# Optimization experiments

Hardware: AMD Instinct MI355X
Metric: run time of the kernel (lower is better)

Reference implementation:

```python
import jax, jax.numpy as jnp
import numpy as np

H_IN = 1024
H_OUT = 1024
P = 512
DT_MIN = 0.004
DT_MAX = 0.1
STEP_RESCALE = 1.0
MIN_NEG = 1e-3
EPS_LAM = 1e-6
EPS_DIV = 1e-9
CLIP_MAX = 20.0


def _hippo_lambda_raw(p):
    # Mirrors TorchS5.__init__ HiPPO-LegS-style symmetric init.
    idx = np.arange(p, dtype=np.float64)
    Pv = np.sqrt(1.0 + 2.0 * idx)
    A = np.tril(Pv[:, None] * Pv[None, :]) - np.diag(idx)
    A = -A
    Pr = np.sqrt(idx + 0.5)
    S = A + Pr[:, None] * Pr[None, :]
    S_sym = 0.5 * (S + S.T)
    eig = np.linalg.eigvalsh(S_sym).astype(np.float32)
    lambda_init = -np.clip(np.abs(eig), 1e-3, None)
    raw = -np.log(np.expm1(np.clip(-lambda_init, 1e-6, None)))
    return jnp.asarray(raw, dtype=jnp.float32)


def setup_inputs() -> dict:
    key = jax.random.key(0)
    ku, kt, kb, kc = jax.random.split(key, 4)
    Bsz, L = 16, 1024
    u = jax.random.normal(ku, (Bsz, L, H_IN), dtype=jnp.float32)
    timesteps = jax.random.uniform(kt, (Bsz, L), dtype=jnp.float32)
    Lambda_raw = _hippo_lambda_raw(P)
    log_step_init = 0.5 * (np.log(DT_MIN) + np.log(DT_MAX))
    log_step = jnp.full((P,), log_step_init, dtype=jnp.float32)
    # kaiming_uniform_(a=sqrt(5)) -> U(-1/sqrt(fan_in), 1/sqrt(fan_in))
    Bmat = jax.random.uniform(kb, (P, H_IN), dtype=jnp.float32,
                              minval=-1.0, maxval=1.0) / np.sqrt(H_IN)
    Cmat = jax.random.uniform(kc, (H_OUT, P), dtype=jnp.float32,
                              minval=-1.0, maxval=1.0) / np.sqrt(P)
    Dvec = jnp.zeros((H_IN,), dtype=jnp.float32)  # H_in == H_out path
    return {"u": u, "timesteps": timesteps, "Lambda_raw": Lambda_raw,
            "log_step": log_step, "B": Bmat, "C": Cmat, "D": Dvec}


def reference(u, timesteps, Lambda_raw, log_step, B, C, D):
    # u: [B,L,H_in], timesteps: [B,L]
    Bu = jnp.einsum('ph,blh->blp', B, u)                      # [B,L,P]
    step_vec = STEP_RESCALE * jnp.exp(log_step)               # [P]
    Lam = -(jax.nn.softplus(Lambda_raw) + MIN_NEG)            # [P]
    Delta = jnp.maximum(step_vec[None, None, :] * timesteps[..., None], 0.0)
    A_bar = jnp.exp(jnp.minimum(Lam[None, None, :] * Delta, CLIP_MAX))
    # zoh gamma: (exp(Lam*Delta)-1)/Lam, fallback Delta near Lam=0
    gamma = jnp.where(jnp.abs(Lam)[None, None, :] > EPS_LAM,
                      (A_bar - 1.0) / Lam[None, None, :], Delta)
    b_seq = gamma * Bu
    A_cum = jnp.cumprod(A_bar, axis=1)                        # [B,L,P]
    z = b_seq / (A_cum + EPS_DIV)
    s = jnp.cumsum(z, axis=1)
    x_seq = A_cum * s
    ys = jnp.einsum('hp,blp->blh', C, x_seq) + D * u          # [B,L,H_out]
    return ys
```

## Files before the change

kernel.cpp:

```cpp
#include <hip/hip_runtime.h>
#include <cstdint>
#include <cstddef>

#define H_IN   1024
#define H_OUTD 1024
#define PDIM   512
#define BSZ    16
#define LSEQ   1024
#define BLM    (BSZ * LSEQ)
#define CCH    32
#define CLEN   32

typedef __bf16 bf16_t;
typedef __bf16 bf16x8 __attribute__((ext_vector_type(8)));
typedef float  floatx4 __attribute__((ext_vector_type(4)));

__device__ __forceinline__ unsigned short f2bf(float f) {
    unsigned u = __float_as_uint(f);
    u = u + 0x7fffu + ((u >> 16) & 1u);
    return (unsigned short)(u >> 16);
}
__device__ __forceinline__ float bf2f(unsigned short s) {
    return __uint_as_float((unsigned)s << 16);
}

__device__ __forceinline__ void gl_lds16(const void* g, void* l) {
    __builtin_amdgcn_global_load_lds(
        (const __attribute__((address_space(1))) void*)g,
        (__attribute__((address_space(3))) void*)l, 16, 0, 0);
}

__global__ void setup_kernel(const float* __restrict__ Lraw,
                             const float* __restrict__ lstep,
                             float* __restrict__ stepv,
                             float* __restrict__ lamv,
                             const float4* __restrict__ Bsrc,
                             ushort4* __restrict__ Bdst,
                             const float4* __restrict__ Csrc,
                             ushort4* __restrict__ Cdst) {
    const int gid = blockIdx.x * 256 + threadIdx.x;
    if (gid < PDIM) {
        stepv[gid] = expf(lstep[gid]);
        float x = Lraw[gid];
        float sp = fmaxf(x, 0.0f) + log1pf(expf(-fabsf(x)));
        lamv[gid] = -(sp + 1e-3f);
    }
    const int nB = PDIM * H_IN / 4;
    if (gid < nB) {
        float4 v = Bsrc[gid];
        ushort4 o;
        o.x = f2bf(v.x); o.y = f2bf(v.y); o.z = f2bf(v.z); o.w = f2bf(v.w);
        Bdst[gid] = o;
    } else {
        const int g2 = gid - nB;
        float4 v = Csrc[g2];
        ushort4 o;
        o.x = f2bf(v.x); o.y = f2bf(v.y); o.z = f2bf(v.z); o.w = f2bf(v.w);
        Cdst[g2] = o;
    }
}

__global__ void cvt_kernel(const float4* __restrict__ src,
                           ushort4* __restrict__ dst, int n4) {
    int i = blockIdx.x * blockDim.x + threadIdx.x;
    if (i < n4) {
        float4 v = src[i];
        ushort4 o;
        o.x = f2bf(v.x); o.y = f2bf(v.y); o.z = f2bf(v.z); o.w = f2bf(v.w);
        dst[i] = o;
    }
}

template<int EPI, int OUTBF>
__global__ __launch_bounds__(256, 4)
void gemm_nt(const bf16_t* __restrict__ A, const bf16_t* __restrict__ Bm,
             float* __restrict__ Cf, unsigned short* __restrict__ Cb,
             int M, int N, int K,
             const float* __restrict__ Dv, const unsigned short* __restrict__ U) {
    __shared__ bf16_t As[128 * 32];
    __shared__ bf16_t Bs[128 * 32];

    const int tid  = threadIdx.x;
    const int lane = tid & 63;
    const int w    = tid >> 6;
    const int m0   = blockIdx.y << 7;
    const int n0   = blockIdx.x << 7;
    const int wm   = (w & 1) << 6;
    const int wn   = (w >> 1) << 6;
    const int r16  = lane & 15;
    const int q    = lane >> 4;
    const int fsw  = (q ^ (r16 & 3)) << 3;

    const int srow = lane >> 2;
    const int seg  = (lane & 3) ^ (srow & 3);
    const int c0   = w * 32;
    const int c1   = c0 + 16;

    const bf16_t* gA0 = A  + (size_t)(m0 + c0 + srow) * K + seg * 8;
    const bf16_t* gA1 = A  + (size_t)(m0 + c1 + srow) * K + seg * 8;
    const bf16_t* gB0 = Bm + (size_t)(n0 + c0 + srow) * K + seg * 8;
    const bf16_t* gB1 = Bm + (size_t)(n0 + c1 + srow) * K + seg * 8;
    bf16_t* lA0 = &As[c0 * 32];
    bf16_t* lA1 = &As[c1 * 32];
    bf16_t* lB0 = &Bs[c0 * 32];
    bf16_t* lB1 = &Bs[c1 * 32];

    floatx4 acc[4][4] = {};

    for (int k0 = 0; k0 < K; k0 += 32) {
        gl_lds16(gA0 + k0, lA0);
        gl_lds16(gA1 + k0, lA1);
        gl_lds16(gB0 + k0, lB0);
        gl_lds16(gB1 + k0, lB1);
        __syncthreads();

        bf16x8 af[4], bfr[4];
#pragma unroll
        for (int i = 0; i < 4; ++i) {
            af[i]  = *(const bf16x8*)&As[(wm + i * 16 + r16) * 32 + fsw];
            bfr[i] = *(const bf16x8*)&Bs[(wn + i * 16 + r16) * 32 + fsw];
        }
#pragma unroll
        for (int mi = 0; mi < 4; ++mi)
#pragma unroll
            for (int ni = 0; ni < 4; ++ni)
                acc[mi][ni] = __builtin_amdgcn_mfma_f32_16x16x32_bf16(
                    af[mi], bfr[ni], acc[mi][ni], 0, 0, 0);
        __syncthreads();
    }

    float dn[4];
    if (EPI == 1) {
#pragma unroll
        for (int ni = 0; ni < 4; ++ni) dn[ni] = Dv[n0 + wn + ni * 16 + r16];
    }
#pragma unroll
    for (int mi = 0; mi < 4; ++mi) {
#pragma unroll
        for (int e = 0; e < 4; ++e) {
            const int m = m0 + wm + mi * 16 + q * 4 + e;
#pragma unroll
            for (int ni = 0; ni < 4; ++ni) {
                const int n = n0 + wn + ni * 16 + r16;
                const size_t idx = (size_t)m * N + n;
                float v = acc[mi][ni][e];
                if (EPI == 1) v += dn[ni] * bf2f(U[idx]);
                if (OUTBF == 1) Cb[idx] = f2bf(v);
                else            Cf[idx] = v;
            }
        }
    }
}

__global__ __launch_bounds__(512)
void scan_part1(const unsigned short* __restrict__ Bu, const float* __restrict__ ts,
                const float* __restrict__ stepv, const float* __restrict__ lamv,
                float* __restrict__ Pagg, float* __restrict__ Sagg) {
    const int c = blockIdx.x;
    const int b = blockIdx.y;
    const int p = threadIdx.x;

    const float lam  = lamv[p];
    const float stp  = stepv[p];
    const float rlam = 1.0f / lam;
    const bool  lam_big = fabsf(lam) > 1e-6f;

    const unsigned short* bu = Bu + ((size_t)b * LSEQ + c * CLEN) * PDIM + p;
    const float* tb = ts + b * LSEQ + c * CLEN;

    float P = 1.0f, S = 0.0f;
#pragma unroll 8
    for (int i = 0; i < CLEN; ++i) {
        float t     = tb[i];
        float delta = fmaxf(stp * t, 0.0f);
        float e     = fminf(lam * delta, 20.0f);
        float abar  = __expf(e);
        float gamma = lam_big ? (abar - 1.0f) * rlam : delta;
        S = fmaf(abar, S, gamma * bf2f(bu[(size_t)i * PDIM]));
        P *= abar;
    }
    const size_t o = ((size_t)b * CCH + c) * PDIM + p;
    Pagg[o] = P;
    Sagg[o] = S;
}

__global__ __launch_bounds__(256)
void scan_chunk(const float* __restrict__ Pagg, const float* __restrict__ Sagg,
                float* __restrict__ X0) {
    const int gid = blockIdx.x * 256 + threadIdx.x;
    const int b   = gid >> 9;
    const int p   = gid & 511;

    float x = 0.0f;
#pragma unroll 8
    for (int c = 0; c < CCH; ++c) {
        const size_t o = ((size_t)b * CCH + c) * PDIM + p;
        X0[o] = x;
        x = fmaf(Pagg[o], x, Sagg[o]);
    }
}

__global__ __launch_bounds__(512)
void scan_part3(const unsigned short* __restrict__ Bu, const float* __restrict__ ts,
                const float* __restrict__ stepv, const float* __restrict__ lamv,
                const float* __restrict__ X0, unsigned short* __restrict__ Xbf) {
    const int c = blockIdx.x;
    const int b = blockIdx.y;
    const int p = threadIdx.x;

    const float lam  = lamv[p];
    const float stp  = stepv[p];
    const float rlam = 1.0f / lam;
    const bool  lam_big = fabsf(lam) > 1e-6f;

    const unsigned short* bu = Bu + ((size_t)b * LSEQ + c * CLEN) * PDIM + p;
    const float* tb = ts + b * LSEQ + c * CLEN;
    unsigned short* xo = Xbf + ((size_t)b * LSEQ + c * CLEN) * PDIM + p;

    float x = X0[((size_t)b * CCH + c) * PDIM + p];
#pragma unroll 8
    for (int i = 0; i < CLEN; ++i) {
        float t     = tb[i];
        float delta = fmaxf(stp * t, 0.0f);
        float e     = fminf(lam * delta, 20.0f);
        float abar  = __expf(e);
        float gamma = lam_big ? (abar - 1.0f) * rlam : delta;
        x = fmaf(abar, x, gamma * bf2f(bu[(size_t)i * PDIM]));
        xo[(size_t)i * PDIM] = f2bf(x);
    }
}

extern "C" void kernel_launch(void* const* d_in, const int* in_sizes, int n_in,
                              void* d_out, int out_size, void* d_ws, size_t ws_size,
                              hipStream_t stream) {
    (void)in_sizes; (void)n_in; (void)out_size; (void)ws_size;
    const float* u  = (const float*)d_in[0];
    const float* ts = (const float*)d_in[1];
    const float* Lr = (const float*)d_in[2];
    const float* ls = (const float*)d_in[3];
    const float* Bm = (const float*)d_in[4];
    const float* Cm = (const float*)d_in[5];
    const float* Dv = (const float*)d_in[6];
    float* out = (float*)d_out;

    char* ws = (char*)d_ws;
    bf16_t*         u_bf = (bf16_t*)(ws);
    bf16_t*         B_bf = (bf16_t*)(ws + (32u << 20));
    bf16_t*         C_bf = (bf16_t*)(ws + (33u << 20));
    unsigned short* Bu   = (unsigned short*)(ws + (34u << 20));
    unsigned short* X_bf = (unsigned short*)(ws + (50u << 20));
    float*          Pagg = (float*)(ws + (66u << 20));
    float*          Sagg = (float*)(ws + (67u << 20));
    float*          X0   = (float*)(ws + (68u << 20));
    float*          stepv= (float*)(ws + (69u << 20));
    float*          lamv = stepv + PDIM;

    setup_kernel<<<1024, 256, 0, stream>>>(Lr, ls, stepv, lamv,
                                           (const float4*)Bm, (ushort4*)B_bf,
                                           (const float4*)Cm, (ushort4*)C_bf);

    cvt_kernel<<<BLM * H_IN / 4 / 256, 256, 0, stream>>>(
        (const float4*)u, (ushort4*)u_bf, BLM * H_IN / 4);

    gemm_nt<0, 1><<<dim3(PDIM / 128, BLM / 128), 256, 0, stream>>>(
        u_bf, B_bf, nullptr, Bu, BLM, PDIM, H_IN, nullptr, nullptr);

    scan_part1<<<dim3(CCH, BSZ), 512, 0, stream>>>(Bu, ts, stepv, lamv, Pagg, Sagg);
    scan_chunk<<<BSZ * PDIM / 256, 256, 0, stream>>>(Pagg, Sagg, X0);
    scan_part3<<<dim3(CCH, BSZ), 512, 0, stream>>>(Bu, ts, stepv, lamv, X0, X_bf);

    gemm_nt<1, 0><<<dim3(H_OUTD / 128, BLM / 128), 256, 0, stream>>>(
        (const bf16_t*)X_bf, C_bf, out, nullptr, BLM, H_OUTD, PDIM, Dv,
        (const unsigned short*)u_bf);
}
```

Measured before the change: 204.1 us.

## Fuse input conversion into setup, merge chunk scan into part3, swizzle GEMM blocks

Converts u, B and C to bf16 in a single setup kernel instead of two launches. The separate chunk-carry kernel is removed: each part3 block recomputes its starting state by serially folding the Pagg/Sagg aggregates of all preceding chunks. Both GEMMs switch to a 1D grid with a grouped block mapping, so neighbouring blocks share A/B tiles in cache. Together these cut launch overhead and the X0 round trip, at the cost of redundant prefix work (up to 31 reads per thread) in later chunks.

```diff
diff --git a/kernel.cpp b/kernel.cpp
--- a/kernel.cpp
+++ b/kernel.cpp
@@ -30,10 +30,15 @@
         (__attribute__((address_space(3))) void*)l, 16, 0, 0);
 }
 
+#define NU4 (BLM * H_IN / 4)
+#define NB4 (PDIM * H_IN / 4)
+#define NC4 (H_OUTD * PDIM / 4)
 __global__ void setup_kernel(const float* __restrict__ Lraw,
                              const float* __restrict__ lstep,
                              float* __restrict__ stepv,
                              float* __restrict__ lamv,
+                             const float4* __restrict__ Usrc,
+                             ushort4* __restrict__ Udst,
                              const float4* __restrict__ Bsrc,
                              ushort4* __restrict__ Bdst,
                              const float4* __restrict__ Csrc,
@@ -45,33 +50,29 @@
         float sp = fmaxf(x, 0.0f) + log1pf(expf(-fabsf(x)));
         lamv[gid] = -(sp + 1e-3f);
     }
-    const int nB = PDIM * H_IN / 4;
-    if (gid < nB) {
-        float4 v = Bsrc[gid];
+    if (gid < NU4) {
+        float4 v = Usrc[gid];
         ushort4 o;
         o.x = f2bf(v.x); o.y = f2bf(v.y); o.z = f2bf(v.z); o.w = f2bf(v.w);
-        Bdst[gid] = o;
+        Udst[gid] = o;
     } else {
-        const int g2 = gid - nB;
-        float4 v = Csrc[g2];
-        ushort4 o;
-        o.x = f2bf(v.x); o.y = f2bf(v.y); o.z = f2bf(v.z); o.w = f2bf(v.w);
-        Cdst[g2] = o;
-    }
-}
-
-__global__ void cvt_kernel(const float4* __restrict__ src,
-                           ushort4* __restrict__ dst, int n4) {
-    int i = blockIdx.x * blockDim.x + threadIdx.x;
-    if (i < n4) {
-        float4 v = src[i];
-        ushort4 o;
-        o.x = f2bf(v.x); o.y = f2bf(v.y); o.z = f2bf(v.z); o.w = f2bf(v.w);
-        dst[i] = o;
-    }
-}
-
-template<int EPI, int OUTBF>
+        const int g2 = gid - NU4;
+        if (g2 < NB4) {
+            float4 v = Bsrc[g2];
+            ushort4 o;
+            o.x = f2bf(v.x); o.y = f2bf(v.y); o.z = f2bf(v.z); o.w = f2bf(v.w);
+            Bdst[g2] = o;
+        } else if (g2 < NB4 + NC4) {
+            const int g3 = g2 - NB4;
+            float4 v = Csrc[g3];
+            ushort4 o;
+            o.x = f2bf(v.x); o.y = f2bf(v.y); o.z = f2bf(v.z); o.w = f2bf(v.w);
+            Cdst[g3] = o;
+        }
+    }
+}
+
+template<int EPI, int OUTBF, int GXL>
 __global__ __launch_bounds__(256, 4)
 void gemm_nt(const bf16_t* __restrict__ A, const bf16_t* __restrict__ Bm,
              float* __restrict__ Cf, unsigned short* __restrict__ Cb,
@@ -80,11 +81,15 @@
     __shared__ bf16_t As[128 * 32];
     __shared__ bf16_t Bs[128 * 32];
 
+    const int i     = blockIdx.x;
+    const int n_blk = (i >> 3) & ((1 << GXL) - 1);
+    const int m_blk = ((i >> (3 + GXL)) << 3) | (i & 7);
+    const int m0    = m_blk << 7;
+    const int n0    = n_blk << 7;
+
     const int tid  = threadIdx.x;
     const int lane = tid & 63;
     const int w    = tid >> 6;
-    const int m0   = blockIdx.y << 7;
-    const int n0   = blockIdx.x << 7;
     const int wm   = (w & 1) << 6;
     const int wn   = (w >> 1) << 6;
     const int r16  = lane & 15;
@@ -116,9 +121,9 @@
 
         bf16x8 af[4], bfr[4];
 #pragma unroll
-        for (int i = 0; i < 4; ++i) {
-            af[i]  = *(const bf16x8*)&As[(wm + i * 16 + r16) * 32 + fsw];
-            bfr[i] = *(const bf16x8*)&Bs[(wn + i * 16 + r16) * 32 + fsw];
+        for (int ii = 0; ii < 4; ++ii) {
+            af[ii]  = *(const bf16x8*)&As[(wm + ii * 16 + r16) * 32 + fsw];
+            bfr[ii] = *(const bf16x8*)&Bs[(wn + ii * 16 + r16) * 32 + fsw];
         }
 #pragma unroll
         for (int mi = 0; mi < 4; ++mi)
@@ -184,26 +189,11 @@
     Sagg[o] = S;
 }
 
-__global__ __launch_bounds__(256)
-void scan_chunk(const float* __restrict__ Pagg, const float* __restrict__ Sagg,
-                float* __restrict__ X0) {
-    const int gid = blockIdx.x * 256 + threadIdx.x;
-    const int b   = gid >> 9;
-    const int p   = gid & 511;
-
-    float x = 0.0f;
-#pragma unroll 8
-    for (int c = 0; c < CCH; ++c) {
-        const size_t o = ((size_t)b * CCH + c) * PDIM + p;
-        X0[o] = x;
-        x = fmaf(Pagg[o], x, Sagg[o]);
-    }
-}
-
 __global__ __launch_bounds__(512)
-void scan_part3(const unsigned short* __restrict__ Bu, const float* __restrict__ ts,
-                const float* __restrict__ stepv, const float* __restrict__ lamv,
-                const float* __restrict__ X0, unsigned short* __restrict__ Xbf) {
+void scan_part23(const unsigned short* __restrict__ Bu, const float* __restrict__ ts,
+                 const float* __restrict__ stepv, const float* __restrict__ lamv,
+                 const float* __restrict__ Pagg, const float* __restrict__ Sagg,
+                 unsigned short* __restrict__ Xbf) {
     const int c = blockIdx.x;
     const int b = blockIdx.y;
     const int p = threadIdx.x;
@@ -213,11 +203,16 @@
     const float rlam = 1.0f / lam;
     const bool  lam_big = fabsf(lam) > 1e-6f;
 
+    float x = 0.0f;
+    for (int cc = 0; cc < c; ++cc) {
+        const size_t o = ((size_t)b * CCH + cc) * PDIM + p;
+        x = fmaf(Pagg[o], x, Sagg[o]);
+    }
+
     const unsigned short* bu = Bu + ((size_t)b * LSEQ + c * CLEN) * PDIM + p;
     const float* tb = ts + b * LSEQ + c * CLEN;
     unsigned short* xo = Xbf + ((size_t)b * LSEQ + c * CLEN) * PDIM + p;
 
-    float x = X0[((size_t)b * CCH + c) * PDIM + p];
 #pragma unroll 8
     for (int i = 0; i < CLEN; ++i) {
         float t     = tb[i];
@@ -251,25 +246,23 @@
     unsigned short* X_bf = (unsigned short*)(ws + (50u << 20));
     float*          Pagg = (float*)(ws + (66u << 20));
     float*          Sagg = (float*)(ws + (67u << 20));
-    float*          X0   = (float*)(ws + (68u << 20));
     float*          stepv= (float*)(ws + (69u << 20));
     float*          lamv = stepv + PDIM;
 
-    setup_kernel<<<1024, 256, 0, stream>>>(Lr, ls, stepv, lamv,
-                                           (const float4*)Bm, (ushort4*)B_bf,
-                                           (const float4*)Cm, (ushort4*)C_bf);
-
-    cvt_kernel<<<BLM * H_IN / 4 / 256, 256, 0, stream>>>(
-        (const float4*)u, (ushort4*)u_bf, BLM * H_IN / 4);
-
-    gemm_nt<0, 1><<<dim3(PDIM / 128, BLM / 128), 256, 0, stream>>>(
+    setup_kernel<<<(NU4 + NB4 + NC4) / 256, 256, 0, stream>>>(
+        Lr, ls, stepv, lamv,
+        (const float4*)u,  (ushort4*)u_bf,
+        (const float4*)Bm, (ushort4*)B_bf,
+        (const float4*)Cm, (ushort4*)C_bf);
+
+    gemm_nt<0, 1, 2><<<512, 256, 0, stream>>>(
         u_bf, B_bf, nullptr, Bu, BLM, PDIM, H_IN, nullptr, nullptr);
 
     scan_part1<<<dim3(CCH, BSZ), 512, 0, stream>>>(Bu, ts, stepv, lamv, Pagg, Sagg);
-    scan_chunk<<<BSZ * PDIM / 256, 256, 0, stream>>>(Pagg, Sagg, X0);
-    scan_part3<<<dim3(CCH, BSZ), 512, 0, stream>>>(Bu, ts, stepv, lamv, X0, X_bf);
-
-    gemm_nt<1, 0><<<dim3(H_OUTD / 128, BLM / 128), 256, 0, stream>>>(
+    scan_part23<<<dim3(CCH, BSZ), 512, 0, stream>>>(Bu, ts, stepv, lamv,
+                                                    Pagg, Sagg, X_bf);
+
+    gemm_nt<1, 0, 3><<<1024, 256, 0, stream>>>(
         (const bf16_t*)X_bf, C_bf, out, nullptr, BLM, H_OUTD, PDIM, Dv,
         (const unsigned short*)u_bf);
 }
```

New measurement: 196.8 us. 3.6% less time.
